# Kernel optimization log

Hardware: AMD Instinct MI355X
Metric: run time of the kernel (lower is better)

Reference implementation:

```python
import jax, jax.numpy as jnp
import numpy as np

B, Q, K, H, V = 32, 64, 512, 64, 64
NEG = -1e6


def setup_inputs() -> dict:
    key = jax.random.key(0)
    ks = jax.random.split(key, 7)
    queries = jax.random.normal(ks[0], (B, Q, H), dtype=jnp.float32)
    keys = jax.random.normal(ks[1], (B, K, H), dtype=jnp.float32)
    values = jax.random.normal(ks[2], (B, K, V), dtype=jnp.float32)
    valid_lens = jax.random.randint(ks[3], (B,), 1, K + 1, dtype=jnp.int32)
    # Linear weights stored as (in_features, out_features); x @ W == torch Linear
    Wq = jax.random.normal(ks[4], (H, H), dtype=jnp.float32) / np.sqrt(H)
    Wk = jax.random.normal(ks[5], (H, H), dtype=jnp.float32) / np.sqrt(H)
    wv = jax.random.normal(ks[6], (H,), dtype=jnp.float32) / np.sqrt(H)
    return {"queries": queries, "keys": keys, "values": values,
            "valid_lens": valid_lens, "Wq": Wq, "Wk": Wk, "wv": wv}


def reference(queries, keys, values, valid_lens, Wq, Wk, wv):
    q = jnp.einsum('bqd,dh->bqh', queries, Wq)          # (B,Q,H)
    k = jnp.einsum('bkd,dh->bkh', keys, Wk)             # (B,K,H)
    # additive (Bahdanau) features: (B,Q,K,H) broadcast intermediate
    feats = jnp.tanh(q[:, :, None, :] + k[:, None, :, :])
    scores = jnp.einsum('bqkh,h->bqk', feats, wv)       # (B,Q,K)
    # masked softmax over key axis: positions >= valid_len get -1e6
    mask = jnp.arange(K)[None, :] < valid_lens[:, None]  # (B,K)
    scores = jnp.where(mask[:, None, :], scores, NEG)
    attn = jax.nn.softmax(scores, axis=-1)              # (B,Q,K)
    return jnp.einsum('bqk,bkv->bqv', attn, values)     # (B,Q,V)
```

## Files before the change

kernel.cpp:

```cpp
#include <hip/hip_runtime.h>

#define NEG (-1e6f)

static constexpr int B = 32, Q = 64, K = 512, H = 64, V = 64;
static constexpr float C2LE = 2.8853900817779268f;
static constexpr float L2E  = 1.4426950408889634f;

typedef __attribute__((ext_vector_type(8))) short bf16x8;
typedef __attribute__((ext_vector_type(4))) float f32x4;

__device__ __forceinline__ float fexp2(float x) { return __builtin_amdgcn_exp2f(x); }
__device__ __forceinline__ float frcp(float x)  { return __builtin_amdgcn_rcpf(x); }

__device__ __forceinline__ unsigned short f2bf(float f) {
  union { float f; unsigned u; } v; v.f = f;
  unsigned r = v.u + 0x7fffu + ((v.u >> 16) & 1u);
  return (unsigned short)(r >> 16);
}
__device__ __forceinline__ unsigned pack2bf(float lo, float hi) {
  return (unsigned)f2bf(lo) | ((unsigned)f2bf(hi) << 16);
}

__global__ __launch_bounds__(256) void proj_kernel(
    const float* __restrict__ queries, const float* __restrict__ keys,
    const float* __restrict__ Wq, const float* __restrict__ Wk,
    const float* __restrict__ wv, const int* __restrict__ vlens,
    float* __restrict__ qAR2, unsigned* __restrict__ Ekp)
{
  __shared__ float Wl[64 * 65];
  const int xcd = blockIdx.x & 7, slot = blockIdx.x >> 3;
  const bool isQ = slot < 4;
  const int b = isQ ? (xcd * 4 + slot) : (xcd * 4 + ((slot - 4) >> 3));
  const int kb64 = (slot - 4) & 7;
  const int vlen = vlens[b];
  if (!isQ && kb64 * 64 >= vlen) return;

  const int tid = threadIdx.x, lane = tid & 63;
  const int wave = __builtin_amdgcn_readfirstlane(tid >> 6);
  const float* Wsrc = isQ ? Wq : Wk;
  #pragma unroll
  for (int i = 0; i < 16; ++i) {
    const int idx = tid + i * 256;
    Wl[(idx >> 6) * 65 + (idx & 63)] = Wsrc[idx];
  }
  __syncthreads();

  const int r = lane & 15, g = lane >> 4;
  const int rloc0 = (isQ ? 0 : kb64 * 64) + wave * 16;
  if (!isQ && rloc0 >= vlen) return;
  const float* xbase = isQ ? (queries + ((size_t)b * Q + rloc0) * H)
                           : (keys    + ((size_t)b * K + rloc0) * H);

  bf16x8 afr[2];
  #pragma unroll
  for (int kb = 0; kb < 2; ++kb) {
    const float* px = xbase + (size_t)r * H + kb * 32 + g * 8;
    const float4 x0 = *(const float4*)px;
    const float4 x1 = *(const float4*)(px + 4);
    bf16x8 a;
    a[0]=f2bf(x0.x); a[1]=f2bf(x0.y); a[2]=f2bf(x0.z); a[3]=f2bf(x0.w);
    a[4]=f2bf(x1.x); a[5]=f2bf(x1.y); a[6]=f2bf(x1.z); a[7]=f2bf(x1.w);
    afr[kb] = a;
  }

  #pragma unroll
  for (int t = 0; t < 4; ++t) {
    const int hcol = t * 16 + r;
    f32x4 acc = {0.f, 0.f, 0.f, 0.f};
    #pragma unroll
    for (int kb = 0; kb < 2; ++kb) {
      bf16x8 wfr;
      #pragma unroll
      for (int j = 0; j < 8; ++j)
        wfr[j] = f2bf(Wl[(kb*32 + g*8 + j) * 65 + hcol]);
      acc = isQ ? __builtin_amdgcn_mfma_f32_16x16x32_bf16(afr[kb], wfr, acc, 0, 0, 0)
                : __builtin_amdgcn_mfma_f32_16x16x32_bf16(wfr, afr[kb], acc, 0, 0, 0);
    }
    if (isQ) {
      const float wvv = wv[hcol];
      #pragma unroll
      for (int rr = 0; rr < 4; ++rr) {
        const int qq = rloc0 + g * 4 + rr;
        const float s = fminf(15.f, fmaxf(-15.f, acc[rr])) * C2LE;
        const float rq = fexp2(-s);
        const size_t off = (((size_t)(b*16 + (qq>>2)) * 32 + (hcol>>1)) * 16)
                           + (qq & 3) * 4 + (hcol & 1) * 2;
        *(float2*)(qAR2 + off) = make_float2(-2.f * wvv * rq, rq);
      }
    } else {
      const int k = rloc0 + r;
      float E[4];
      #pragma unroll
      for (int rr = 0; rr < 4; ++rr)
        E[rr] = fexp2(fminf(15.f, fmaxf(-15.f, acc[rr])) * C2LE);
      const int hp = t * 8 + g * 2;
      Ekp[((size_t)b*32 + hp    ) * 512 + k] = pack2bf(E[0], E[1]);
      Ekp[((size_t)b*32 + hp + 1) * 512 + k] = pack2bf(E[2], E[3]);
    }
  }
}

__global__ __launch_bounds__(512) void attn_kernel(
    const float* __restrict__ qAR2, const unsigned* __restrict__ Ekp,
    const float* __restrict__ values, const int* __restrict__ vlens,
    float* __restrict__ out)
{
  __shared__ float p[4][K];
  __shared__ float part[8][4][V];
  __shared__ float red[4][2][2];

  const int xcd = blockIdx.x & 7, slot = blockIdx.x >> 3;
  const int b = xcd * 4 + (slot >> 4), qg = slot & 15;
  const int vlen = vlens[b];
  const int tid = threadIdx.x, lane = tid & 63;
  const int wave = __builtin_amdgcn_readfirstlane(tid >> 6);

  if (wave * 64 < vlen) {
    const unsigned* ekp = Ekp + (size_t)b * 32 * 512 + tid;
    const float* ar = qAR2 +
        (size_t)__builtin_amdgcn_readfirstlane((b * 16 + qg) * 512);
    float a0 = 0.f, a1 = 0.f, a2 = 0.f, a3 = 0.f;
    #pragma unroll
    for (int hp = 0; hp < 32; ++hp) {
      const unsigned u = ekp[hp * 512];
      const float E0 = __uint_as_float(u << 16);
      const float E1 = __uint_as_float(u & 0xffff0000u);
      const float* s = ar + hp * 16;
      a0 = fmaf(s[ 0], frcp(s[ 1] + E0), a0);
      a0 = fmaf(s[ 2], frcp(s[ 3] + E1), a0);
      a1 = fmaf(s[ 4], frcp(s[ 5] + E0), a1);
      a1 = fmaf(s[ 6], frcp(s[ 7] + E1), a1);
      a2 = fmaf(s[ 8], frcp(s[ 9] + E0), a2);
      a2 = fmaf(s[10], frcp(s[11] + E1), a2);
      a3 = fmaf(s[12], frcp(s[13] + E0), a3);
      a3 = fmaf(s[14], frcp(s[15] + E1), a3);
    }
    p[0][tid] = a0; p[1][tid] = a1; p[2][tid] = a2; p[3][tid] = a3;
  }
  __syncthreads();

  const int qi = wave & 3, half = wave >> 2;
  const int kb2 = half * 256 + lane * 4;
  {
    float s[4];
    *(float4*)s = *(const float4*)&p[qi][kb2];
    float m = NEG;
    #pragma unroll
    for (int j = 0; j < 4; ++j) {
      s[j] = (kb2 + j < vlen) ? s[j] : NEG;
      m = fmaxf(m, s[j]);
    }
    #pragma unroll
    for (int off = 32; off; off >>= 1) m = fmaxf(m, __shfl_xor(m, off, 64));
    if (lane == 0) red[qi][half][0] = m;
    __syncthreads();
    m = fmaxf(red[qi][0][0], red[qi][1][0]);
    float sum = 0.f;
    #pragma unroll
    for (int j = 0; j < 4; ++j) { s[j] = fexp2((s[j] - m) * L2E); sum += s[j]; }
    *(float4*)&p[qi][kb2] = *(float4*)s;
    #pragma unroll
    for (int off = 32; off; off >>= 1) sum += __shfl_xor(sum, off, 64);
    if (lane == 0) red[qi][half][1] = sum;
    __syncthreads();
  }

  {
    const int kb = wave * 64;
    if (kb < vlen) {
      const float* vb = values + ((size_t)b * K + kb) * V + lane;
      float a0 = 0.f, a1 = 0.f, a2 = 0.f, a3 = 0.f;
      #pragma unroll 4
      for (int k4 = 0; k4 < 64; k4 += 4) {
        const float4 p0 = *(const float4*)&p[0][kb + k4];
        const float4 p1 = *(const float4*)&p[1][kb + k4];
        const float4 p2 = *(const float4*)&p[2][kb + k4];
        const float4 p3 = *(const float4*)&p[3][kb + k4];
        const float v0 = vb[(size_t)(k4 + 0) * V];
        const float v1 = vb[(size_t)(k4 + 1) * V];
        const float v2 = vb[(size_t)(k4 + 2) * V];
        const float v3 = vb[(size_t)(k4 + 3) * V];
        a0 = fmaf(p0.x,v0, fmaf(p0.y,v1, fmaf(p0.z,v2, fmaf(p0.w,v3, a0))));
        a1 = fmaf(p1.x,v0, fmaf(p1.y,v1, fmaf(p1.z,v2, fmaf(p1.w,v3, a1))));
        a2 = fmaf(p2.x,v0, fmaf(p2.y,v1, fmaf(p2.z,v2, fmaf(p2.w,v3, a2))));
        a3 = fmaf(p3.x,v0, fmaf(p3.y,v1, fmaf(p3.z,v2, fmaf(p3.w,v3, a3))));
      }
      part[wave][0][lane] = a0; part[wave][1][lane] = a1;
      part[wave][2][lane] = a2; part[wave][3][lane] = a3;
    } else {
      part[wave][0][lane] = 0.f; part[wave][1][lane] = 0.f;
      part[wave][2][lane] = 0.f; part[wave][3][lane] = 0.f;
    }
  }
  __syncthreads();

  if (wave < 4) {
    const float inv = frcp(red[wave][0][1] + red[wave][1][1]);
    float o = 0.f;
    #pragma unroll
    for (int w = 0; w < 8; ++w) o += part[w][wave][lane];
    out[((size_t)b * Q + qg * 4 + wave) * V + lane] = o * inv;
  }
}

extern "C" void kernel_launch(void* const* d_in, const int* in_sizes, int n_in,
                              void* d_out, int out_size, void* d_ws, size_t ws_size,
                              hipStream_t stream) {
  const float* queries = (const float*)d_in[0];
  const float* keys    = (const float*)d_in[1];
  const float* values  = (const float*)d_in[2];
  const int*   vlens   = (const int*)d_in[3];
  const float* Wq      = (const float*)d_in[4];
  const float* Wk      = (const float*)d_in[5];
  const float* wv      = (const float*)d_in[6];
  float* out = (float*)d_out;

  float*    qAR2 = (float*)d_ws;
  unsigned* Ekp  = (unsigned*)(qAR2 + (size_t)B*16*32*16);

  proj_kernel<<<288, 256, 0, stream>>>(queries, keys, Wq, Wk, wv, vlens, qAR2, Ekp);
  attn_kernel<<<512, 512, 0, stream>>>(qAR2, Ekp, values, vlens, out);
}
```

Baseline: 23.50 us.

## Halve queries per attention block to double grid and preload Ek into registers

The attention kernel now processes 2 queries per block instead of 4, doubling the grid to 1024 blocks. The qAR2 layout and the softmax reduction (now four key quarters) are reorganised to match. The 32 packed Ek loads are hoisted into a register array before the compute loop, and the projection kernel's block-to-batch mapping is interleaved. This aims to raise parallelism and latency hiding, at the cost of reloading Ek and values twice as often per batch.

```diff
diff --git a/kernel.cpp b/kernel.cpp
--- a/kernel.cpp
+++ b/kernel.cpp
@@ -30,8 +30,9 @@
   __shared__ float Wl[64 * 65];
   const int xcd = blockIdx.x & 7, slot = blockIdx.x >> 3;
   const bool isQ = slot < 4;
-  const int b = isQ ? (xcd * 4 + slot) : (xcd * 4 + ((slot - 4) >> 3));
-  const int kb64 = (slot - 4) & 7;
+  const int idx = slot - 4;
+  const int b = isQ ? (xcd * 4 + slot) : (xcd * 4 + (idx & 3));
+  const int kb64 = idx >> 2;
   const int vlen = vlens[b];
   if (!isQ && kb64 * 64 >= vlen) return;
 
@@ -40,8 +41,8 @@
   const float* Wsrc = isQ ? Wq : Wk;
   #pragma unroll
   for (int i = 0; i < 16; ++i) {
-    const int idx = tid + i * 256;
-    Wl[(idx >> 6) * 65 + (idx & 63)] = Wsrc[idx];
+    const int j = tid + i * 256;
+    Wl[(j >> 6) * 65 + (j & 63)] = Wsrc[j];
   }
   __syncthreads();
 
@@ -58,8 +59,8 @@
     const float4 x0 = *(const float4*)px;
     const float4 x1 = *(const float4*)(px + 4);
     bf16x8 a;
-    a[0]=f2bf(x0.x); a[1]=f2bf(x0.y); a[2]=f2bf(x0.z); a[3]=f2bf(x0.w);
-    a[4]=f2bf(x1.x); a[5]=f2bf(x1.y); a[6]=f2bf(x1.z); a[7]=f2bf(x1.w);
+    a[0]=(short)f2bf(x0.x); a[1]=(short)f2bf(x0.y); a[2]=(short)f2bf(x0.z); a[3]=(short)f2bf(x0.w);
+    a[4]=(short)f2bf(x1.x); a[5]=(short)f2bf(x1.y); a[6]=(short)f2bf(x1.z); a[7]=(short)f2bf(x1.w);
     afr[kb] = a;
   }
 
@@ -72,7 +73,7 @@
       bf16x8 wfr;
       #pragma unroll
       for (int j = 0; j < 8; ++j)
-        wfr[j] = f2bf(Wl[(kb*32 + g*8 + j) * 65 + hcol]);
+        wfr[j] = (short)f2bf(Wl[(kb*32 + g*8 + j) * 65 + hcol]);
       acc = isQ ? __builtin_amdgcn_mfma_f32_16x16x32_bf16(afr[kb], wfr, acc, 0, 0, 0)
                 : __builtin_amdgcn_mfma_f32_16x16x32_bf16(wfr, afr[kb], acc, 0, 0, 0);
     }
@@ -83,8 +84,8 @@
         const int qq = rloc0 + g * 4 + rr;
         const float s = fminf(15.f, fmaxf(-15.f, acc[rr])) * C2LE;
         const float rq = fexp2(-s);
-        const size_t off = (((size_t)(b*16 + (qq>>2)) * 32 + (hcol>>1)) * 16)
-                           + (qq & 3) * 4 + (hcol & 1) * 2;
+        const size_t off = (((size_t)(b * 32 + (qq >> 1)) * 32 + (hcol >> 1)) * 8)
+                           + (qq & 1) * 4 + (hcol & 1) * 2;
         *(float2*)(qAR2 + off) = make_float2(-2.f * wvv * rq, rq);
       }
     } else {
@@ -105,12 +106,12 @@
     const float* __restrict__ values, const int* __restrict__ vlens,
     float* __restrict__ out)
 {
-  __shared__ float p[4][K];
-  __shared__ float part[8][4][V];
-  __shared__ float red[4][2][2];
+  __shared__ float p[2][K];
+  __shared__ float part[8][2][V];
+  __shared__ float red[2][4][2];
 
   const int xcd = blockIdx.x & 7, slot = blockIdx.x >> 3;
-  const int b = xcd * 4 + (slot >> 4), qg = slot & 15;
+  const int b = xcd * 4 + (slot & 3), qg = slot >> 2;
   const int vlen = vlens[b];
   const int tid = threadIdx.x, lane = tid & 63;
   const int wave = __builtin_amdgcn_readfirstlane(tid >> 6);
@@ -118,50 +119,45 @@
   if (wave * 64 < vlen) {
     const unsigned* ekp = Ekp + (size_t)b * 32 * 512 + tid;
     const float* ar = qAR2 +
-        (size_t)__builtin_amdgcn_readfirstlane((b * 16 + qg) * 512);
-    float a0 = 0.f, a1 = 0.f, a2 = 0.f, a3 = 0.f;
+        (size_t)__builtin_amdgcn_readfirstlane((b * 32 + qg) * 256);
+    unsigned ek[32];
+    #pragma unroll
+    for (int hp = 0; hp < 32; ++hp) ek[hp] = ekp[hp * 512];
+    float a0 = 0.f, a1 = 0.f;
     #pragma unroll
     for (int hp = 0; hp < 32; ++hp) {
-      const unsigned u = ekp[hp * 512];
-      const float E0 = __uint_as_float(u << 16);
-      const float E1 = __uint_as_float(u & 0xffff0000u);
-      const float* s = ar + hp * 16;
-      a0 = fmaf(s[ 0], frcp(s[ 1] + E0), a0);
-      a0 = fmaf(s[ 2], frcp(s[ 3] + E1), a0);
-      a1 = fmaf(s[ 4], frcp(s[ 5] + E0), a1);
-      a1 = fmaf(s[ 6], frcp(s[ 7] + E1), a1);
-      a2 = fmaf(s[ 8], frcp(s[ 9] + E0), a2);
-      a2 = fmaf(s[10], frcp(s[11] + E1), a2);
-      a3 = fmaf(s[12], frcp(s[13] + E0), a3);
-      a3 = fmaf(s[14], frcp(s[15] + E1), a3);
-    }
-    p[0][tid] = a0; p[1][tid] = a1; p[2][tid] = a2; p[3][tid] = a3;
+      const float E0 = __uint_as_float(ek[hp] << 16);
+      const float E1 = __uint_as_float(ek[hp] & 0xffff0000u);
+      const float* s = ar + hp * 8;
+      a0 = fmaf(s[0], frcp(s[1] + E0), a0);
+      a0 = fmaf(s[2], frcp(s[3] + E1), a0);
+      a1 = fmaf(s[4], frcp(s[5] + E0), a1);
+      a1 = fmaf(s[6], frcp(s[7] + E1), a1);
+    }
+    p[0][tid] = a0; p[1][tid] = a1;
   }
   __syncthreads();
 
-  const int qi = wave & 3, half = wave >> 2;
-  const int kb2 = half * 256 + lane * 4;
+  const int qi = wave & 1, quarter = wave >> 1;
+  const int kb2 = quarter * 128 + lane * 2;
   {
-    float s[4];
-    *(float4*)s = *(const float4*)&p[qi][kb2];
-    float m = NEG;
-    #pragma unroll
-    for (int j = 0; j < 4; ++j) {
-      s[j] = (kb2 + j < vlen) ? s[j] : NEG;
-      m = fmaxf(m, s[j]);
-    }
+    float2 s = *(const float2*)&p[qi][kb2];
+    s.x = (kb2     < vlen) ? s.x : NEG;
+    s.y = (kb2 + 1 < vlen) ? s.y : NEG;
+    float m = fmaxf(s.x, s.y);
     #pragma unroll
     for (int off = 32; off; off >>= 1) m = fmaxf(m, __shfl_xor(m, off, 64));
-    if (lane == 0) red[qi][half][0] = m;
+    if (lane == 0) red[qi][quarter][0] = m;
     __syncthreads();
-    m = fmaxf(red[qi][0][0], red[qi][1][0]);
-    float sum = 0.f;
-    #pragma unroll
-    for (int j = 0; j < 4; ++j) { s[j] = fexp2((s[j] - m) * L2E); sum += s[j]; }
-    *(float4*)&p[qi][kb2] = *(float4*)s;
+    m = fmaxf(fmaxf(red[qi][0][0], red[qi][1][0]),
+              fmaxf(red[qi][2][0], red[qi][3][0]));
+    s.x = fexp2((s.x - m) * L2E);
+    s.y = fexp2((s.y - m) * L2E);
+    *(float2*)&p[qi][kb2] = s;
+    float sum = s.x + s.y;
     #pragma unroll
     for (int off = 32; off; off >>= 1) sum += __shfl_xor(sum, off, 64);
-    if (lane == 0) red[qi][half][1] = sum;
+    if (lane == 0) red[qi][quarter][1] = sum;
     __syncthreads();
   }
 
@@ -169,37 +165,32 @@
     const int kb = wave * 64;
     if (kb < vlen) {
       const float* vb = values + ((size_t)b * K + kb) * V + lane;
-      float a0 = 0.f, a1 = 0.f, a2 = 0.f, a3 = 0.f;
+      float a0 = 0.f, a1 = 0.f;
       #pragma unroll 4
       for (int k4 = 0; k4 < 64; k4 += 4) {
         const float4 p0 = *(const float4*)&p[0][kb + k4];
         const float4 p1 = *(const float4*)&p[1][kb + k4];
-        const float4 p2 = *(const float4*)&p[2][kb + k4];
-        const float4 p3 = *(const float4*)&p[3][kb + k4];
         const float v0 = vb[(size_t)(k4 + 0) * V];
         const float v1 = vb[(size_t)(k4 + 1) * V];
         const float v2 = vb[(size_t)(k4 + 2) * V];
         const float v3 = vb[(size_t)(k4 + 3) * V];
         a0 = fmaf(p0.x,v0, fmaf(p0.y,v1, fmaf(p0.z,v2, fmaf(p0.w,v3, a0))));
         a1 = fmaf(p1.x,v0, fmaf(p1.y,v1, fmaf(p1.z,v2, fmaf(p1.w,v3, a1))));
-        a2 = fmaf(p2.x,v0, fmaf(p2.y,v1, fmaf(p2.z,v2, fmaf(p2.w,v3, a2))));
-        a3 = fmaf(p3.x,v0, fmaf(p3.y,v1, fmaf(p3.z,v2, fmaf(p3.w,v3, a3))));
       }
       part[wave][0][lane] = a0; part[wave][1][lane] = a1;
-      part[wave][2][lane] = a2; part[wave][3][lane] = a3;
     } else {
       part[wave][0][lane] = 0.f; part[wave][1][lane] = 0.f;
-      part[wave][2][lane] = 0.f; part[wave][3][lane] = 0.f;
     }
   }
   __syncthreads();
 
-  if (wave < 4) {
-    const float inv = frcp(red[wave][0][1] + red[wave][1][1]);
+  if (wave < 2) {
+    const float inv = frcp(red[wave][0][1] + red[wave][1][1] +
+                           red[wave][2][1] + red[wave][3][1]);
     float o = 0.f;
     #pragma unroll
     for (int w = 0; w < 8; ++w) o += part[w][wave][lane];
-    out[((size_t)b * Q + qg * 4 + wave) * V + lane] = o * inv;
+    out[((size_t)b * Q + qg * 2 + wave) * V + lane] = o * inv;
   }
 }
 
@@ -216,8 +207,8 @@
   float* out = (float*)d_out;
 
   float*    qAR2 = (float*)d_ws;
-  unsigned* Ekp  = (unsigned*)(qAR2 + (size_t)B*16*32*16);
+  unsigned* Ekp  = (unsigned*)(qAR2 + (size_t)B*32*256);
 
   proj_kernel<<<288, 256, 0, stream>>>(queries, keys, Wq, Wk, wv, vlens, qAR2, Ekp);
-  attn_kernel<<<512, 512, 0, stream>>>(qAR2, Ekp, values, vlens, out);
-}
+  attn_kernel<<<1024, 512, 0, stream>>>(qAR2, Ekp, values, vlens, out);
+}
```

After: 24.15 us. 2.8% more time.

## Fuse projection and attention kernels, recomputing key projections per block in LDS

Applied to the files above, without the earlier changes.

Merges the projection kernel and the attention kernel into one launch. Each block now computes the key projection for its batch and keeps the packed exp values in shared memory instead of a global workspace, and it computes its own query-group coefficients. This removes a kernel launch and the global round trip of the key intermediate. In exchange, every one of the 16 blocks per batch redundantly reloads and projects all valid keys, and a 64KB LDS buffer limits occupancy.

```diff
diff --git a/kernel.cpp b/kernel.cpp
--- a/kernel.cpp
+++ b/kernel.cpp
@@ -21,121 +21,110 @@
   return (unsigned)f2bf(lo) | ((unsigned)f2bf(hi) << 16);
 }
 
-__global__ __launch_bounds__(256) void proj_kernel(
+__global__ __launch_bounds__(512) void fused_kernel(
     const float* __restrict__ queries, const float* __restrict__ keys,
+    const float* __restrict__ values, const int* __restrict__ vlens,
     const float* __restrict__ Wq, const float* __restrict__ Wk,
-    const float* __restrict__ wv, const int* __restrict__ vlens,
-    float* __restrict__ qAR2, unsigned* __restrict__ Ekp)
+    const float* __restrict__ wv,
+    float* __restrict__ qar_ws, float* __restrict__ out)
 {
-  __shared__ float Wl[64 * 65];
-  const int xcd = blockIdx.x & 7, slot = blockIdx.x >> 3;
-  const bool isQ = slot < 4;
-  const int b = isQ ? (xcd * 4 + slot) : (xcd * 4 + ((slot - 4) >> 3));
-  const int kb64 = (slot - 4) & 7;
-  const int vlen = vlens[b];
-  if (!isQ && kb64 * 64 >= vlen) return;
+  __shared__ unsigned ekl[32][512];
+  __shared__ float red[4][2][2];
 
   const int tid = threadIdx.x, lane = tid & 63;
   const int wave = __builtin_amdgcn_readfirstlane(tid >> 6);
-  const float* Wsrc = isQ ? Wq : Wk;
-  #pragma unroll
-  for (int i = 0; i < 16; ++i) {
-    const int idx = tid + i * 256;
-    Wl[(idx >> 6) * 65 + (idx & 63)] = Wsrc[idx];
-  }
-  __syncthreads();
-
+  const int xcd = blockIdx.x & 7, sub = blockIdx.x >> 3;
+  const int b = xcd * 4 + (sub & 3), qg = sub >> 2;
+  const int vlen = vlens[b];
   const int r = lane & 15, g = lane >> 4;
-  const int rloc0 = (isQ ? 0 : kb64 * 64) + wave * 16;
-  if (!isQ && rloc0 >= vlen) return;
-  const float* xbase = isQ ? (queries + ((size_t)b * Q + rloc0) * H)
-                           : (keys    + ((size_t)b * K + rloc0) * H);
-
-  bf16x8 afr[2];
-  #pragma unroll
-  for (int kb = 0; kb < 2; ++kb) {
-    const float* px = xbase + (size_t)r * H + kb * 32 + g * 8;
-    const float4 x0 = *(const float4*)px;
-    const float4 x1 = *(const float4*)(px + 4);
-    bf16x8 a;
-    a[0]=f2bf(x0.x); a[1]=f2bf(x0.y); a[2]=f2bf(x0.z); a[3]=f2bf(x0.w);
-    a[4]=f2bf(x1.x); a[5]=f2bf(x1.y); a[6]=f2bf(x1.z); a[7]=f2bf(x1.w);
-    afr[kb] = a;
-  }
-
-  #pragma unroll
-  for (int t = 0; t < 4; ++t) {
-    const int hcol = t * 16 + r;
+  const int t = wave & 3;
+
+  if (wave < 4) {
+    const float* px = queries + ((size_t)b * Q + (qg >> 2) * 16 + r) * H;
+    const int hcol = wave * 16 + r;
     f32x4 acc = {0.f, 0.f, 0.f, 0.f};
     #pragma unroll
     for (int kb = 0; kb < 2; ++kb) {
-      bf16x8 wfr;
+      const float4 x0 = *(const float4*)(px + kb * 32 + g * 8);
+      const float4 x1 = *(const float4*)(px + kb * 32 + g * 8 + 4);
+      bf16x8 afr, wfr;
+      afr[0]=(short)f2bf(x0.x); afr[1]=(short)f2bf(x0.y); afr[2]=(short)f2bf(x0.z); afr[3]=(short)f2bf(x0.w);
+      afr[4]=(short)f2bf(x1.x); afr[5]=(short)f2bf(x1.y); afr[6]=(short)f2bf(x1.z); afr[7]=(short)f2bf(x1.w);
       #pragma unroll
       for (int j = 0; j < 8; ++j)
-        wfr[j] = f2bf(Wl[(kb*32 + g*8 + j) * 65 + hcol]);
-      acc = isQ ? __builtin_amdgcn_mfma_f32_16x16x32_bf16(afr[kb], wfr, acc, 0, 0, 0)
-                : __builtin_amdgcn_mfma_f32_16x16x32_bf16(wfr, afr[kb], acc, 0, 0, 0);
-    }
-    if (isQ) {
+        wfr[j] = (short)f2bf(Wq[(kb * 32 + g * 8 + j) * H + hcol]);
+      acc = __builtin_amdgcn_mfma_f32_16x16x32_bf16(afr, wfr, acc, 0, 0, 0);
+    }
+    if (g == (qg & 3)) {
       const float wvv = wv[hcol];
+      float* dst = qar_ws + ((size_t)(b * 16 + qg) * 32 + (hcol >> 1)) * 16
+                          + (hcol & 1) * 2;
       #pragma unroll
       for (int rr = 0; rr < 4; ++rr) {
-        const int qq = rloc0 + g * 4 + rr;
         const float s = fminf(15.f, fmaxf(-15.f, acc[rr])) * C2LE;
         const float rq = fexp2(-s);
-        const size_t off = (((size_t)(b*16 + (qq>>2)) * 32 + (hcol>>1)) * 16)
-                           + (qq & 3) * 4 + (hcol & 1) * 2;
-        *(float2*)(qAR2 + off) = make_float2(-2.f * wvv * rq, rq);
+        *(float2*)(dst + rr * 4) = make_float2(-2.f * wvv * rq, rq);
       }
-    } else {
-      const int k = rloc0 + r;
+    }
+  }
+
+  {
+    bf16x8 wk[2];
+    #pragma unroll
+    for (int kb = 0; kb < 2; ++kb)
+      #pragma unroll
+      for (int j = 0; j < 8; ++j)
+        wk[kb][j] = (short)f2bf(Wk[(kb * 32 + g * 8 + j) * H + t * 16 + r]);
+
+    const int nstr = (vlen + 15) >> 4;
+    for (int s = (wave >> 2); s < nstr; s += 2) {
+      const float* px = keys + ((size_t)b * K + s * 16 + r) * H;
+      f32x4 acc = {0.f, 0.f, 0.f, 0.f};
+      #pragma unroll
+      for (int kb = 0; kb < 2; ++kb) {
+        const float4 x0 = *(const float4*)(px + kb * 32 + g * 8);
+        const float4 x1 = *(const float4*)(px + kb * 32 + g * 8 + 4);
+        bf16x8 afr;
+        afr[0]=(short)f2bf(x0.x); afr[1]=(short)f2bf(x0.y); afr[2]=(short)f2bf(x0.z); afr[3]=(short)f2bf(x0.w);
+        afr[4]=(short)f2bf(x1.x); afr[5]=(short)f2bf(x1.y); afr[6]=(short)f2bf(x1.z); afr[7]=(short)f2bf(x1.w);
+        acc = __builtin_amdgcn_mfma_f32_16x16x32_bf16(wk[kb], afr, acc, 0, 0, 0);
+      }
       float E[4];
       #pragma unroll
       for (int rr = 0; rr < 4; ++rr)
         E[rr] = fexp2(fminf(15.f, fmaxf(-15.f, acc[rr])) * C2LE);
+      const int k = s * 16 + r;
       const int hp = t * 8 + g * 2;
-      Ekp[((size_t)b*32 + hp    ) * 512 + k] = pack2bf(E[0], E[1]);
-      Ekp[((size_t)b*32 + hp + 1) * 512 + k] = pack2bf(E[2], E[3]);
-    }
-  }
-}
-
-__global__ __launch_bounds__(512) void attn_kernel(
-    const float* __restrict__ qAR2, const unsigned* __restrict__ Ekp,
-    const float* __restrict__ values, const int* __restrict__ vlens,
-    float* __restrict__ out)
-{
-  __shared__ float p[4][K];
-  __shared__ float part[8][4][V];
-  __shared__ float red[4][2][2];
-
-  const int xcd = blockIdx.x & 7, slot = blockIdx.x >> 3;
-  const int b = xcd * 4 + (slot >> 4), qg = slot & 15;
-  const int vlen = vlens[b];
-  const int tid = threadIdx.x, lane = tid & 63;
-  const int wave = __builtin_amdgcn_readfirstlane(tid >> 6);
-
+      ekl[hp][k]     = pack2bf(E[0], E[1]);
+      ekl[hp + 1][k] = pack2bf(E[2], E[3]);
+    }
+  }
+  __syncthreads();
+
+  float a0 = 0.f, a1 = 0.f, a2 = 0.f, a3 = 0.f;
   if (wave * 64 < vlen) {
-    const unsigned* ekp = Ekp + (size_t)b * 32 * 512 + tid;
-    const float* ar = qAR2 +
-        (size_t)__builtin_amdgcn_readfirstlane((b * 16 + qg) * 512);
-    float a0 = 0.f, a1 = 0.f, a2 = 0.f, a3 = 0.f;
+    const float* arp = qar_ws + (size_t)(b * 16 + qg) * 512;
     #pragma unroll
     for (int hp = 0; hp < 32; ++hp) {
-      const unsigned u = ekp[hp * 512];
+      const unsigned u = ekl[hp][tid];
       const float E0 = __uint_as_float(u << 16);
       const float E1 = __uint_as_float(u & 0xffff0000u);
-      const float* s = ar + hp * 16;
-      a0 = fmaf(s[ 0], frcp(s[ 1] + E0), a0);
-      a0 = fmaf(s[ 2], frcp(s[ 3] + E1), a0);
-      a1 = fmaf(s[ 4], frcp(s[ 5] + E0), a1);
-      a1 = fmaf(s[ 6], frcp(s[ 7] + E1), a1);
-      a2 = fmaf(s[ 8], frcp(s[ 9] + E0), a2);
-      a2 = fmaf(s[10], frcp(s[11] + E1), a2);
-      a3 = fmaf(s[12], frcp(s[13] + E0), a3);
-      a3 = fmaf(s[14], frcp(s[15] + E1), a3);
-    }
-    p[0][tid] = a0; p[1][tid] = a1; p[2][tid] = a2; p[3][tid] = a3;
+      const float4 s0 = *(const float4*)(arp + hp * 16 + 0);
+      const float4 s1 = *(const float4*)(arp + hp * 16 + 4);
+      const float4 s2 = *(const float4*)(arp + hp * 16 + 8);
+      const float4 s3 = *(const float4*)(arp + hp * 16 + 12);
+      a0 = fmaf(s0.x, frcp(s0.y + E0), a0); a0 = fmaf(s0.z, frcp(s0.w + E1), a0);
+      a1 = fmaf(s1.x, frcp(s1.y + E0), a1); a1 = fmaf(s1.z, frcp(s1.w + E1), a1);
+      a2 = fmaf(s2.x, frcp(s2.y + E0), a2); a2 = fmaf(s2.z, frcp(s2.w + E1), a2);
+      a3 = fmaf(s3.x, frcp(s3.y + E0), a3); a3 = fmaf(s3.z, frcp(s3.w + E1), a3);
+    }
+  }
+  __syncthreads();
+  float* p    = (float*)ekl;
+  float* part = (float*)ekl + 4 * 512;
+  if (wave * 64 < vlen) {
+    p[0 * 512 + tid] = a0; p[1 * 512 + tid] = a1;
+    p[2 * 512 + tid] = a2; p[3 * 512 + tid] = a3;
   }
   __syncthreads();
 
@@ -143,7 +132,7 @@
   const int kb2 = half * 256 + lane * 4;
   {
     float s[4];
-    *(float4*)s = *(const float4*)&p[qi][kb2];
+    *(float4*)s = *(const float4*)&p[qi * 512 + kb2];
     float m = NEG;
     #pragma unroll
     for (int j = 0; j < 4; ++j) {
@@ -158,7 +147,7 @@
     float sum = 0.f;
     #pragma unroll
     for (int j = 0; j < 4; ++j) { s[j] = fexp2((s[j] - m) * L2E); sum += s[j]; }
-    *(float4*)&p[qi][kb2] = *(float4*)s;
+    *(float4*)&p[qi * 512 + kb2] = *(float4*)s;
     #pragma unroll
     for (int off = 32; off; off >>= 1) sum += __shfl_xor(sum, off, 64);
     if (lane == 0) red[qi][half][1] = sum;
@@ -169,27 +158,27 @@
     const int kb = wave * 64;
     if (kb < vlen) {
       const float* vb = values + ((size_t)b * K + kb) * V + lane;
-      float a0 = 0.f, a1 = 0.f, a2 = 0.f, a3 = 0.f;
+      float c0 = 0.f, c1 = 0.f, c2 = 0.f, c3 = 0.f;
       #pragma unroll 4
       for (int k4 = 0; k4 < 64; k4 += 4) {
-        const float4 p0 = *(const float4*)&p[0][kb + k4];
-        const float4 p1 = *(const float4*)&p[1][kb + k4];
-        const float4 p2 = *(const float4*)&p[2][kb + k4];
-        const float4 p3 = *(const float4*)&p[3][kb + k4];
+        const float4 p0 = *(const float4*)&p[0 * 512 + kb + k4];
+        const float4 p1 = *(const float4*)&p[1 * 512 + kb + k4];
+        const float4 p2 = *(const float4*)&p[2 * 512 + kb + k4];
+        const float4 p3 = *(const float4*)&p[3 * 512 + kb + k4];
         const float v0 = vb[(size_t)(k4 + 0) * V];
         const float v1 = vb[(size_t)(k4 + 1) * V];
         const float v2 = vb[(size_t)(k4 + 2) * V];
         const float v3 = vb[(size_t)(k4 + 3) * V];
-        a0 = fmaf(p0.x,v0, fmaf(p0.y,v1, fmaf(p0.z,v2, fmaf(p0.w,v3, a0))));
-        a1 = fmaf(p1.x,v0, fmaf(p1.y,v1, fmaf(p1.z,v2, fmaf(p1.w,v3, a1))));
-        a2 = fmaf(p2.x,v0, fmaf(p2.y,v1, fmaf(p2.z,v2, fmaf(p2.w,v3, a2))));
-        a3 = fmaf(p3.x,v0, fmaf(p3.y,v1, fmaf(p3.z,v2, fmaf(p3.w,v3, a3))));
+        c0 = fmaf(p0.x,v0, fmaf(p0.y,v1, fmaf(p0.z,v2, fmaf(p0.w,v3, c0))));
+        c1 = fmaf(p1.x,v0, fmaf(p1.y,v1, fmaf(p1.z,v2, fmaf(p1.w,v3, c1))));
+        c2 = fmaf(p2.x,v0, fmaf(p2.y,v1, fmaf(p2.z,v2, fmaf(p2.w,v3, c2))));
+        c3 = fmaf(p3.x,v0, fmaf(p3.y,v1, fmaf(p3.z,v2, fmaf(p3.w,v3, c3))));
       }
-      part[wave][0][lane] = a0; part[wave][1][lane] = a1;
-      part[wave][2][lane] = a2; part[wave][3][lane] = a3;
+      part[(wave*4+0)*64+lane] = c0; part[(wave*4+1)*64+lane] = c1;
+      part[(wave*4+2)*64+lane] = c2; part[(wave*4+3)*64+lane] = c3;
     } else {
-      part[wave][0][lane] = 0.f; part[wave][1][lane] = 0.f;
-      part[wave][2][lane] = 0.f; part[wave][3][lane] = 0.f;
+      part[(wave*4+0)*64+lane] = 0.f; part[(wave*4+1)*64+lane] = 0.f;
+      part[(wave*4+2)*64+lane] = 0.f; part[(wave*4+3)*64+lane] = 0.f;
     }
   }
   __syncthreads();
@@ -198,7 +187,7 @@
     const float inv = frcp(red[wave][0][1] + red[wave][1][1]);
     float o = 0.f;
     #pragma unroll
-    for (int w = 0; w < 8; ++w) o += part[w][wave][lane];
+    for (int w = 0; w < 8; ++w) o += part[(w*4+wave)*64 + lane];
     out[((size_t)b * Q + qg * 4 + wave) * V + lane] = o * inv;
   }
 }
@@ -214,10 +203,8 @@
   const float* Wk      = (const float*)d_in[5];
   const float* wv      = (const float*)d_in[6];
   float* out = (float*)d_out;
-
-  float*    qAR2 = (float*)d_ws;
-  unsigned* Ekp  = (unsigned*)(qAR2 + (size_t)B*16*32*16);
-
-  proj_kernel<<<288, 256, 0, stream>>>(queries, keys, Wq, Wk, wv, vlens, qAR2, Ekp);
-  attn_kernel<<<512, 512, 0, stream>>>(qAR2, Ekp, values, vlens, out);
-}
+  float* qar_ws = (float*)d_ws;
+
+  fused_kernel<<<512, 512, 0, stream>>>(queries, keys, values, vlens,
+                                        Wq, Wk, wv, qar_ws, out);
+}
```

After: 57.45 us. +144.5%, slower.
